# Kernel tuning notes

Measured on AMD Instinct MI355X. Metric: run time of the kernel, lower is better.

## Reference

```python
import math
import jax, jax.numpy as jnp
import numpy as np

B, T, D = 8, 2048, 512
EPS = 1e-5


def _gate(x, W, b, a, g, beta):
    # Linear -> PReLU (single shared slope a) -> LayerNorm -> sigmoid
    h = x @ W.T + b
    h = jnp.where(h >= 0, h, a * h)
    mu = jnp.mean(h, axis=-1, keepdims=True)
    var = jnp.var(h, axis=-1, keepdims=True)
    h = (h - mu) / jnp.sqrt(var + EPS) * g + beta
    return jax.nn.sigmoid(h)


def setup_inputs() -> dict:
    key = jax.random.key(0)
    ks = jax.random.split(key, 12)
    lin = lambda k: jax.random.normal(k, (D, D), jnp.float32) * 0.02
    z = jnp.zeros((D,), jnp.float32)
    o = jnp.ones((D,), jnp.float32)
    a0 = jnp.float32(0.25)  # PReLU default init
    inp = {
        "query": jax.random.normal(ks[0], (B, T, D), jnp.float32),
        "value": jax.random.normal(ks[1], (B, T, D), jnp.float32),
        "aux_emb": jax.random.normal(ks[2], (B, 1, D), jnp.float32),
        # ragged valid lengths in [T//2, T] to keep every sample realistic
        "input_len": jax.random.randint(ks[3], (B,), T // 2, T + 1),
        "Wq": lin(ks[4]), "bq": z,
        "Wqg": lin(ks[5]), "bqg": z, "aq": a0, "gq": o, "betaq": z,
        "Wkg": lin(ks[6]), "bkg": z, "ak": a0, "gk": o, "betak": z,
        "Wvg": lin(ks[7]), "bvg": z, "av": a0, "gv": o, "betav": z,
        "Wsig": lin(ks[8]), "bsig": z,
        "Wtan": lin(ks[9]), "btan": z,
    }
    return inp


def reference(query, value, aux_emb, input_len,
              Wq, bq,
              Wqg, bqg, aq, gq, betaq,
              Wkg, bkg, ak, gk, betak,
              Wvg, bvg, av, gv, betav,
              Wsig, bsig, Wtan, btan):
    q = query @ Wq.T + bq
    q = q * _gate(aux_emb, Wqg, bqg, aq, gq, betaq)          # [B,T,D]
    k = value * _gate(aux_emb, Wkg, bkg, ak, gk, betak)      # [B,T,D]
    vg = _gate(aux_emb, Wvg, bvg, av, gv, betav)             # [B,1,D]
    vg = jax.nn.sigmoid(vg @ Wsig.T + bsig) * jnp.tanh(vg @ Wtan.T + btan)
    v = value * vg                                           # [B,T,D]

    w = jnp.einsum('btd,bsd->bts', q, k) / math.sqrt(D)      # [B,T,T]
    r = jnp.arange(T)
    causal = (r[:, None] >= r[None, :]).astype(w.dtype)      # tril ones
    w = w * causal
    w = jnp.where(w == 0.0, -jnp.inf, w)  # torch quirk: exact zeros -> -inf
    L = input_len[:, None, None]                              # [B,1,1]
    invalid = (r[None, :, None] < L) & (r[None, None, :] >= L)
    w = jnp.where(invalid, -jnp.inf, w)
    p = jax.nn.softmax(w, axis=-1)
    # rows beyond input_len are padding: zero them (torch code produced NaN
    # there via -inf*0; intended semantics is zeroed padding rows)
    row_valid = (r[None, :, None] < L).astype(p.dtype)        # [B,T,1]
    p = p * row_valid
    return p @ v                                              # [B,T,D]
```

## Files before the change

kernel.cpp:

```cpp
#include <hip/hip_runtime.h>
#include <hip/hip_bf16.h>
#include <stdint.h>

#define BB 8
#define TT 2048
#define DD 512

typedef __attribute__((ext_vector_type(8))) __bf16 bf16x8;
typedef __attribute__((ext_vector_type(4))) float f32x4;
typedef __attribute__((ext_vector_type(8))) unsigned short ushort8_t;

__device__ __forceinline__ unsigned short f2bf(float f) {
    unsigned u = __builtin_bit_cast(unsigned, f);
    unsigned r = u + 0x7fffu + ((u >> 16) & 1u);
    return (unsigned short)(r >> 16);
}

__device__ __forceinline__ void gload_lds16(const unsigned short* g, unsigned short* l) {
    __builtin_amdgcn_global_load_lds(
        (const __attribute__((address_space(1))) void*)g,
        (__attribute__((address_space(3))) void*)l, 16, 0, 0);
}

__global__ __launch_bounds__(256) void gates_mv1(
    const float* __restrict__ aux,
    const float* __restrict__ Wqg, const float* __restrict__ bqg, const float* __restrict__ aq,
    const float* __restrict__ Wkg, const float* __restrict__ bkg, const float* __restrict__ ak,
    const float* __restrict__ Wvg, const float* __restrict__ bvg, const float* __restrict__ av,
    float* __restrict__ h) {
    __shared__ float saux[BB * DD];
    int tid = threadIdx.x;
#pragma unroll
    for (int i = 0; i < 4; i++) {
        int idx = tid + i * 256;
        ((float4*)saux)[idx] = ((const float4*)aux)[idx];
    }
    __syncthreads();
    int wave = (blockIdx.x * 256 + tid) >> 6;
    int lane = tid & 63;
    int g = wave >> 9, r = wave & 511;
    const float* W    = (g == 0) ? Wqg : (g == 1) ? Wkg : Wvg;
    const float* bias = (g == 0) ? bqg : (g == 1) ? bkg : bvg;
    const float* alpha = (g == 0) ? aq : (g == 1) ? ak : av;
    const float4* Wrow = (const float4*)(W + (size_t)r * DD);
    float acc[BB];
#pragma unroll
    for (int b = 0; b < BB; b++) acc[b] = 0.f;
#pragma unroll
    for (int c = 0; c < 2; c++) {
        float4 w4 = Wrow[lane + c * 64];
#pragma unroll
        for (int b = 0; b < BB; b++) {
            float4 a4 = ((const float4*)(saux + b * DD))[lane + c * 64];
            acc[b] += w4.x * a4.x + w4.y * a4.y + w4.z * a4.z + w4.w * a4.w;
        }
    }
#pragma unroll
    for (int b = 0; b < BB; b++) {
#pragma unroll
        for (int s = 1; s < 64; s <<= 1) acc[b] += __shfl_xor(acc[b], s, 64);
    }
    if (lane == 0) {
        float bi = bias[r], a = alpha[0];
#pragma unroll
        for (int b = 0; b < BB; b++) {
            float v = acc[b] + bi;
            v = (v >= 0.f) ? v : a * v;
            h[(g * BB + b) * DD + r] = v;
        }
    }
}

__global__ __launch_bounds__(512) void gates_norm(
    const float* __restrict__ h,
    const float* __restrict__ gq, const float* __restrict__ betaq,
    const float* __restrict__ gk, const float* __restrict__ betak,
    const float* __restrict__ gv, const float* __restrict__ betav,
    float* __restrict__ qgate, float* __restrict__ kgate, float* __restrict__ vg) {
    int g = blockIdx.x >> 3, b = blockIdx.x & 7, tid = threadIdx.x;
    __shared__ float red[DD], red2[DD];
    float hv = h[(g * BB + b) * DD + tid];
    red[tid] = hv; red2[tid] = hv * hv;
    __syncthreads();
    for (int s = 256; s > 0; s >>= 1) {
        if (tid < s) { red[tid] += red[tid + s]; red2[tid] += red2[tid + s]; }
        __syncthreads();
    }
    float mu = red[0] * (1.f / DD);
    float var = red2[0] * (1.f / DD) - mu * mu;
    const float* gg = (g == 0) ? gq : (g == 1) ? gk : gv;
    const float* be = (g == 0) ? betaq : (g == 1) ? betak : betav;
    float val = (hv - mu) * rsqrtf(var + 1e-5f) * gg[tid] + be[tid];
    float sg = 1.f / (1.f + expf(-val));
    float* outp = (g == 0) ? qgate : (g == 1) ? kgate : vg;
    outp[b * DD + tid] = sg;
}

__global__ __launch_bounds__(256) void gates_mv2(
    const float* __restrict__ vg,
    const float* __restrict__ Wsig, const float* __restrict__ bsig,
    const float* __restrict__ Wtan, const float* __restrict__ btan,
    float* __restrict__ vgate) {
    __shared__ float svg[BB * DD];
    int tid = threadIdx.x;
#pragma unroll
    for (int i = 0; i < 4; i++) {
        int idx = tid + i * 256;
        ((float4*)svg)[idx] = ((const float4*)vg)[idx];
    }
    __syncthreads();
    int r = (blockIdx.x * 256 + tid) >> 6;
    int lane = tid & 63;
    const float4* Ws = (const float4*)(Wsig + (size_t)r * DD);
    const float4* Wt = (const float4*)(Wtan + (size_t)r * DD);
    float as_[BB], at_[BB];
#pragma unroll
    for (int b = 0; b < BB; b++) { as_[b] = 0.f; at_[b] = 0.f; }
#pragma unroll
    for (int c = 0; c < 2; c++) {
        float4 w1 = Ws[lane + c * 64];
        float4 w2 = Wt[lane + c * 64];
#pragma unroll
        for (int b = 0; b < BB; b++) {
            float4 a4 = ((const float4*)(svg + b * DD))[lane + c * 64];
            as_[b] += w1.x * a4.x + w1.y * a4.y + w1.z * a4.z + w1.w * a4.w;
            at_[b] += w2.x * a4.x + w2.y * a4.y + w2.z * a4.z + w2.w * a4.w;
        }
    }
#pragma unroll
    for (int b = 0; b < BB; b++) {
#pragma unroll
        for (int s = 1; s < 64; s <<= 1) {
            as_[b] += __shfl_xor(as_[b], s, 64);
            at_[b] += __shfl_xor(at_[b], s, 64);
        }
    }
    if (lane == 0) {
        float b1 = bsig[r], b2 = btan[r];
#pragma unroll
        for (int b = 0; b < BB; b++) {
            float s1 = 1.f / (1.f + expf(-(as_[b] + b1)));
            float s2 = tanhf(at_[b] + b2);
            vgate[b * DD + r] = s1 * s2;
        }
    }
}

__global__ __launch_bounds__(256) void convert_kernel(
    const float* __restrict__ query, const float* __restrict__ Wq,
    const float* __restrict__ value,
    const float* __restrict__ kgate, const float* __restrict__ vgate,
    unsigned short* __restrict__ queryb, unsigned short* __restrict__ Wqb,
    unsigned short* __restrict__ kb, unsigned short* __restrict__ vbT) {
    __shared__ float tileF[64][65];
    int bi = blockIdx.x, tid = threadIdx.x;
    if (bi < 8192) {
        int idx = bi * 256 + tid;
        float4 q4 = ((const float4*)query)[idx];
        ushort4 oq;
        oq.x = f2bf(q4.x); oq.y = f2bf(q4.y); oq.z = f2bf(q4.z); oq.w = f2bf(q4.w);
        ((ushort4*)queryb)[idx] = oq;
    } else if (bi < 8448) {
        int idx = (bi - 8192) * 256 + tid;
        float4 w4 = ((const float4*)Wq)[idx];
        ushort4 o;
        o.x = f2bf(w4.x); o.y = f2bf(w4.y); o.z = f2bf(w4.z); o.w = f2bf(w4.w);
        ((ushort4*)Wqb)[idx] = o;
    } else {
        int vb = bi - 8448;
        int tIdx = vb & 31, dIdx = (vb >> 5) & 7, b = vb >> 8;
        int t0 = tIdx * 64, d0 = dIdx * 64;
        int row = tid >> 2;
        int cg = tid & 3;
        float v[16], kgv[16];
        const float* src = &value[((size_t)b * TT + t0 + row) * DD + d0 + cg * 16];
#pragma unroll
        for (int j = 0; j < 4; j++) {
            float4 f = ((const float4*)src)[j];
            v[j * 4 + 0] = f.x; v[j * 4 + 1] = f.y; v[j * 4 + 2] = f.z; v[j * 4 + 3] = f.w;
            float4 g = *(const float4*)&kgate[b * DD + d0 + cg * 16 + j * 4];
            kgv[j * 4 + 0] = g.x; kgv[j * 4 + 1] = g.y; kgv[j * 4 + 2] = g.z; kgv[j * 4 + 3] = g.w;
        }
        ushort8_t kb8[2];
#pragma unroll
        for (int h = 0; h < 2; h++)
#pragma unroll
            for (int j = 0; j < 8; j++)
                kb8[h][j] = f2bf(v[h * 8 + j] * kgv[h * 8 + j]);
        unsigned short* kdst = &kb[((size_t)b * TT + t0 + row) * DD + d0 + cg * 16];
        *(ushort8_t*)&kdst[0] = kb8[0];
        *(ushort8_t*)&kdst[8] = kb8[1];
#pragma unroll
        for (int j = 0; j < 16; j++) tileF[row][cg * 16 + j] = v[j];
        __syncthreads();
        int d = row;
        float g = vgate[b * DD + d0 + d];
        ushort8_t o8[2];
#pragma unroll
        for (int h = 0; h < 2; h++)
#pragma unroll
            for (int j = 0; j < 8; j++)
                o8[h][j] = f2bf(tileF[cg * 16 + h * 8 + j][d] * g);
        unsigned short* vdst = &vbT[((size_t)b * DD + d0 + d) * TT + t0 + cg * 16];
        *(ushort8_t*)&vdst[0] = o8[0];
        *(ushort8_t*)&vdst[8] = o8[1];
    }
}

#define STAGE_AB(BUF, K0)                                                                 \
    _Pragma("unroll") for (int i = 0; i < 2; i++) {                                       \
        int idx = tid * 8 + i * 2048;                                                     \
        int r = idx >> 5;                                                                 \
        int cg = ((idx >> 3) & 3) ^ ((r >> 1) & 3);                                       \
        gload_lds16(&Ap_[(size_t)r * lda_ + (K0) + cg * 8], &As[BUF][idx]);               \
        gload_lds16(&Bp_[(size_t)r * ldb_ + (K0) + cg * 8], &Bs[BUF][idx]);               \
    }

#define GEMM_CORE(APTR, ALDA, BPTR, BLDA, KSTART, KEND)                                   \
    __shared__ __align__(16) unsigned short As[2][128 * 32];                              \
    __shared__ __align__(16) unsigned short Bs[2][128 * 32];                              \
    const unsigned short* Ap_ = (APTR);                                                   \
    const unsigned short* Bp_ = (BPTR);                                                   \
    const int lda_ = (ALDA), ldb_ = (BLDA);                                               \
    int tid = threadIdx.x;                                                                \
    int lane = tid & 63, wid = tid >> 6;                                                  \
    int wm = (wid >> 1) * 64, wn = (wid & 1) * 64;                                        \
    int lm = lane & 15, quad = lane >> 4;                                                 \
    f32x4 acc[4][4];                                                                      \
    _Pragma("unroll") for (int im = 0; im < 4; im++)                                      \
        _Pragma("unroll") for (int in = 0; in < 4; in++)                                  \
            acc[im][in] = (f32x4){0.f, 0.f, 0.f, 0.f};                                    \
    STAGE_AB(0, (KSTART))                                                                 \
    int cur_ = 0;                                                                         \
    for (int k0 = (KSTART); k0 < (KEND); k0 += 32) {                                      \
        __syncthreads();                                                                  \
        if (k0 + 32 < (KEND)) { STAGE_AB(cur_ ^ 1, k0 + 32) }                             \
        bf16x8 af[4], bf_[4];                                                             \
        _Pragma("unroll") for (int i = 0; i < 4; i++) {                                   \
            int row = wm + i * 16 + lm;                                                   \
            af[i] = *(const bf16x8*)&As[cur_][row * 32 + (quad ^ ((row >> 1) & 3)) * 8];  \
        }                                                                                 \
        _Pragma("unroll") for (int i = 0; i < 4; i++) {                                   \
            int row = wn + i * 16 + lm;                                                   \
            bf_[i] = *(const bf16x8*)&Bs[cur_][row * 32 + (quad ^ ((row >> 1) & 3)) * 8]; \
        }                                                                                 \
        _Pragma("unroll") for (int im = 0; im < 4; im++)                                  \
            _Pragma("unroll") for (int in = 0; in < 4; in++)                              \
                acc[im][in] = __builtin_amdgcn_mfma_f32_16x16x32_bf16(af[im], bf_[in],    \
                                                                     acc[im][in], 0, 0, 0);\
        cur_ ^= 1;                                                                        \
    }

__global__ __launch_bounds__(256) void qgemm_kernel(
    const unsigned short* __restrict__ Amat, const unsigned short* __restrict__ Bmat,
    const float* __restrict__ bq, const float* __restrict__ qgate,
    unsigned short* __restrict__ qb) {
    int m0 = blockIdx.x * 128, n0 = blockIdx.y * 128;
    const unsigned short* Ap = Amat + (size_t)m0 * DD;
    const unsigned short* Bp = Bmat + (size_t)n0 * DD;
    GEMM_CORE(Ap, DD, Bp, DD, 0, DD)
    int b = m0 >> 11;
#pragma unroll
    for (int im = 0; im < 4; im++) {
        int row = m0 + wm + im * 16 + quad * 4;
#pragma unroll
        for (int in = 0; in < 4; in++) {
            int col = n0 + wn + in * 16 + lm;
            float bias = bq[col];
            float g = qgate[b * DD + col];
#pragma unroll
            for (int r = 0; r < 4; r++) {
                float v = (acc[im][in][r] + bias) * g;
                qb[(size_t)(row + r) * DD + col] = f2bf(v);
            }
        }
    }
}

__global__ __launch_bounds__(256) void scores_kernel(
    const unsigned short* __restrict__ qb, const unsigned short* __restrict__ kb,
    unsigned short* __restrict__ P, float* __restrict__ rowsum) {
    int b = blockIdx.z;
    int idx = blockIdx.x;
    int mt = (int)((sqrtf(8.f * idx + 1.f) - 1.f) * 0.5f);
    while ((mt + 1) * (mt + 2) / 2 <= idx) mt++;
    while (mt * (mt + 1) / 2 > idx) mt--;
    int nt = idx - mt * (mt + 1) / 2;
    int t0 = mt * 128, s0 = nt * 128;
    const unsigned short* Ap = qb + ((size_t)b * TT + t0) * DD;
    const unsigned short* Bp = kb + ((size_t)b * TT + s0) * DD;
    GEMM_CORE(Ap, DD, Bp, DD, 0, DD)
    const float scale = 0.044194173824159216f;
    unsigned short* Ptile = P + ((size_t)b * 136 + (size_t)mt * (mt + 1) / 2 + nt) * 16384;
#pragma unroll
    for (int im = 0; im < 4; im++) {
        int ltb = wm + im * 16 + quad * 4;
        float rs[4] = {0.f, 0.f, 0.f, 0.f};
#pragma unroll
        for (int in = 0; in < 4; in++) {
            int ls = wn + in * 16 + lm;
            int s = s0 + ls;
#pragma unroll
            for (int r = 0; r < 4; r++) {
                float p = (s <= t0 + ltb + r) ? expf(acc[im][in][r] * scale) : 0.f;
                Ptile[(size_t)(ltb + r) * 128 + ls] = f2bf(p);
                rs[r] += p;
            }
        }
#pragma unroll
        for (int r = 0; r < 4; r++) {
            float v = rs[r];
            v += __shfl_xor(v, 1, 64);
            v += __shfl_xor(v, 2, 64);
            v += __shfl_xor(v, 4, 64);
            v += __shfl_xor(v, 8, 64);
            if (lm == 0) atomicAdd(&rowsum[b * TT + t0 + ltb + r], v);
        }
    }
}

__global__ __launch_bounds__(256) void out_kernel(
    const unsigned short* __restrict__ P, const unsigned short* __restrict__ vbT,
    const float* __restrict__ rowsum, const int* __restrict__ input_len,
    float* __restrict__ out) {
    int lin = blockIdx.x + 4 * blockIdx.y + 64 * blockIdx.z;
    int b = lin & 7;
    int rem = lin >> 3;
    int nt = rem & 3;
    int pr = rem >> 2;
    int n0 = nt * 128;
    int L = input_len[b];

    __shared__ __align__(16) unsigned short As[2][64 * 64];
    __shared__ __align__(16) unsigned short Bs[2][128 * 64];
    int tid = threadIdx.x;
    int lane = tid & 63, wid = tid >> 6;
    int wm = (wid >> 1) * 32, wn = (wid & 1) * 64;
    int lm = lane & 15, quad = lane >> 4;

#pragma unroll
    for (int half = 0; half < 2; half++) {
        int mt = half ? (31 - pr) : pr;
        int t0 = mt * 64;
        int mt128 = mt >> 1;
        int rowoff = (mt & 1) * 64;
        size_t triBase = ((size_t)b * 136 + (size_t)mt128 * (mt128 + 1) / 2) * 16384;
        int ksteps = mt + 1;

        f32x4 acc[2][4];
#pragma unroll
        for (int im = 0; im < 2; im++)
#pragma unroll
            for (int in = 0; in < 4; in++) acc[im][in] = (f32x4){0.f, 0.f, 0.f, 0.f};

#define OUT_STAGE(BUF, KS)                                                              \
        {                                                                               \
            int k0s = (KS) * 64;                                                        \
            int stile = k0s >> 7;                                                       \
            int coloff = k0s & 64;                                                      \
            _Pragma("unroll") for (int i = 0; i < 2; i++) {                             \
                int idx = tid * 8 + i * 2048;                                           \
                int r = idx >> 6;                                                       \
                int c = (idx >> 3) & 7;                                                 \
                int cs = c ^ (r & 7);                                                   \
                const unsigned short* ag = P + triBase + (size_t)stile * 16384 +        \
                                           (size_t)(rowoff + r) * 128 + coloff + cs * 8;\
                gload_lds16(ag, &As[BUF][idx]);                                         \
            }                                                                           \
            _Pragma("unroll") for (int i = 0; i < 4; i++) {                             \
                int idx = tid * 8 + i * 2048;                                           \
                int r = idx >> 6;                                                       \
                int c = (idx >> 3) & 7;                                                 \
                int cs = c ^ (r & 7);                                                   \
                gload_lds16(&vbT[(size_t)(b * DD + n0 + r) * TT + k0s + cs * 8],        \
                            &Bs[BUF][idx]);                                             \
            }                                                                           \
        }

        OUT_STAGE(0, 0)
        int cur = 0;
        for (int ks = 0; ks < ksteps; ks++) {
            __syncthreads();
            if (ks + 1 < ksteps) { OUT_STAGE(cur ^ 1, ks + 1) }
            bf16x8 af[2][2], bf_[4][2];
#pragma unroll
            for (int kk = 0; kk < 2; kk++) {
#pragma unroll
                for (int i = 0; i < 2; i++) {
                    int row = wm + i * 16 + lm;
                    af[i][kk] = *(const bf16x8*)&As[cur][row * 64 + ((kk * 4 + quad) ^ (row & 7)) * 8];
                }
#pragma unroll
                for (int i = 0; i < 4; i++) {
                    int row = wn + i * 16 + lm;
                    bf_[i][kk] = *(const bf16x8*)&Bs[cur][row * 64 + ((kk * 4 + quad) ^ (row & 7)) * 8];
                }
            }
#pragma unroll
            for (int kk = 0; kk < 2; kk++)
#pragma unroll
                for (int im = 0; im < 2; im++)
#pragma unroll
                    for (int in = 0; in < 4; in++)
                        acc[im][in] = __builtin_amdgcn_mfma_f32_16x16x32_bf16(
                            af[im][kk], bf_[in][kk], acc[im][in], 0, 0, 0);
            cur ^= 1;
        }
        __syncthreads();
#undef OUT_STAGE

#pragma unroll
        for (int im = 0; im < 2; im++) {
            int tbase = t0 + wm + im * 16 + quad * 4;
#pragma unroll
            for (int r = 0; r < 4; r++) {
                int t = tbase + r;
                float inv = 1.f / rowsum[b * TT + t];
                bool valid = (t < L);
#pragma unroll
                for (int in = 0; in < 4; in++) {
                    int n = n0 + wn + in * 16 + lm;
                    float o = valid ? acc[im][in][r] * inv : 0.f;
                    out[((size_t)b * TT + t) * DD + n] = o;
                }
            }
        }
    }
}

extern "C" void kernel_launch(void* const* d_in, const int* in_sizes, int n_in,
                              void* d_out, int out_size, void* d_ws, size_t ws_size,
                              hipStream_t stream) {
    const float* query = (const float*)d_in[0];
    const float* value = (const float*)d_in[1];
    const float* aux   = (const float*)d_in[2];
    const int*   ilen  = (const int*)d_in[3];
    const float* Wq    = (const float*)d_in[4];
    const float* bq    = (const float*)d_in[5];
    const float* Wqg   = (const float*)d_in[6];
    const float* bqg   = (const float*)d_in[7];
    const float* aq    = (const float*)d_in[8];
    const float* gq    = (const float*)d_in[9];
    const float* betaq = (const float*)d_in[10];
    const float* Wkg   = (const float*)d_in[11];
    const float* bkg   = (const float*)d_in[12];
    const float* ak    = (const float*)d_in[13];
    const float* gk    = (const float*)d_in[14];
    const float* betak = (const float*)d_in[15];
    const float* Wvg   = (const float*)d_in[16];
    const float* bvg   = (const float*)d_in[17];
    const float* av    = (const float*)d_in[18];
    const float* gv    = (const float*)d_in[19];
    const float* betav = (const float*)d_in[20];
    const float* Wsig  = (const float*)d_in[21];
    const float* bsig  = (const float*)d_in[22];
    const float* Wtan  = (const float*)d_in[23];
    const float* btan  = (const float*)d_in[24];

    char* ws = (char*)d_ws;
    float* qgate          = (float*)(ws + 0);
    float* kgate          = (float*)(ws + 16384);
    float* vgate          = (float*)(ws + 32768);
    float* rowsum         = (float*)(ws + 49152);
    unsigned short* Wqb   = (unsigned short*)(ws + 114688);
    unsigned short* queryb= (unsigned short*)(ws + 638976);
    unsigned short* qb    = (unsigned short*)(ws + 17416192);
    unsigned short* kb    = (unsigned short*)(ws + 34193408);
    unsigned short* vbT   = (unsigned short*)(ws + 50970624);
    unsigned short* P     = (unsigned short*)(ws + 67747840);
    float* hbuf           = (float*)(ws + 67747840);
    float* vg             = (float*)(ws + 67747840 + 49152);

    hipMemsetAsync(rowsum, 0, BB * TT * sizeof(float), stream);

    gates_mv1<<<384, 256, 0, stream>>>(aux, Wqg, bqg, aq, Wkg, bkg, ak, Wvg, bvg, av, hbuf);
    gates_norm<<<24, 512, 0, stream>>>(hbuf, gq, betaq, gk, betak, gv, betav,
                                       qgate, kgate, vg);
    gates_mv2<<<128, 256, 0, stream>>>(vg, Wsig, bsig, Wtan, btan, vgate);

    convert_kernel<<<10496, 256, 0, stream>>>(query, Wq, value, kgate, vgate,
                                              queryb, Wqb, kb, vbT);
    qgemm_kernel<<<dim3((BB * TT) / 128, DD / 128), 256, 0, stream>>>(queryb, Wqb, bq, qgate, qb);
    scores_kernel<<<dim3(136, 1, BB), 256, 0, stream>>>(qb, kb, P, rowsum);
    out_kernel<<<dim3(4, 16, BB), 256, 0, stream>>>(P, vbT, rowsum, ilen, (float*)d_out);
}
```

Before: 274.2 us.

## Fuse gate matvecs, layernorm, and rowsum zeroing into one per-batch kernel

Three gate kernels (matvec, layernorm/sigmoid, second matvec) and the rowsum memset are merged into one kernel with one 512-thread block per batch. Each thread computes a full 512-length dot product for one output row, and results pass between stages through shared memory. This removes three launches and a memset along with their intermediate global round-trips. The cost is only 8 blocks in flight, each thread streaming a whole weight row uncoalesced, and every block re-reading all five weight matrices, which may serialize gate computation.

```diff
diff --git a/kernel.cpp b/kernel.cpp
--- a/kernel.cpp
+++ b/kernel.cpp
@@ -22,128 +22,76 @@
         (__attribute__((address_space(3))) void*)l, 16, 0, 0);
 }
 
-__global__ __launch_bounds__(256) void gates_mv1(
+__global__ __launch_bounds__(512) void gates_fused(
     const float* __restrict__ aux,
     const float* __restrict__ Wqg, const float* __restrict__ bqg, const float* __restrict__ aq,
     const float* __restrict__ Wkg, const float* __restrict__ bkg, const float* __restrict__ ak,
     const float* __restrict__ Wvg, const float* __restrict__ bvg, const float* __restrict__ av,
-    float* __restrict__ h) {
-    __shared__ float saux[BB * DD];
-    int tid = threadIdx.x;
-#pragma unroll
-    for (int i = 0; i < 4; i++) {
-        int idx = tid + i * 256;
-        ((float4*)saux)[idx] = ((const float4*)aux)[idx];
-    }
-    __syncthreads();
-    int wave = (blockIdx.x * 256 + tid) >> 6;
-    int lane = tid & 63;
-    int g = wave >> 9, r = wave & 511;
-    const float* W    = (g == 0) ? Wqg : (g == 1) ? Wkg : Wvg;
-    const float* bias = (g == 0) ? bqg : (g == 1) ? bkg : bvg;
-    const float* alpha = (g == 0) ? aq : (g == 1) ? ak : av;
-    const float4* Wrow = (const float4*)(W + (size_t)r * DD);
-    float acc[BB];
-#pragma unroll
-    for (int b = 0; b < BB; b++) acc[b] = 0.f;
-#pragma unroll
-    for (int c = 0; c < 2; c++) {
-        float4 w4 = Wrow[lane + c * 64];
-#pragma unroll
-        for (int b = 0; b < BB; b++) {
-            float4 a4 = ((const float4*)(saux + b * DD))[lane + c * 64];
-            acc[b] += w4.x * a4.x + w4.y * a4.y + w4.z * a4.z + w4.w * a4.w;
-        }
-    }
-#pragma unroll
-    for (int b = 0; b < BB; b++) {
-#pragma unroll
-        for (int s = 1; s < 64; s <<= 1) acc[b] += __shfl_xor(acc[b], s, 64);
-    }
-    if (lane == 0) {
-        float bi = bias[r], a = alpha[0];
-#pragma unroll
-        for (int b = 0; b < BB; b++) {
-            float v = acc[b] + bi;
-            v = (v >= 0.f) ? v : a * v;
-            h[(g * BB + b) * DD + r] = v;
-        }
-    }
-}
-
-__global__ __launch_bounds__(512) void gates_norm(
-    const float* __restrict__ h,
     const float* __restrict__ gq, const float* __restrict__ betaq,
     const float* __restrict__ gk, const float* __restrict__ betak,
     const float* __restrict__ gv, const float* __restrict__ betav,
-    float* __restrict__ qgate, float* __restrict__ kgate, float* __restrict__ vg) {
-    int g = blockIdx.x >> 3, b = blockIdx.x & 7, tid = threadIdx.x;
-    __shared__ float red[DD], red2[DD];
-    float hv = h[(g * BB + b) * DD + tid];
-    red[tid] = hv; red2[tid] = hv * hv;
-    __syncthreads();
-    for (int s = 256; s > 0; s >>= 1) {
-        if (tid < s) { red[tid] += red[tid + s]; red2[tid] += red2[tid + s]; }
-        __syncthreads();
-    }
-    float mu = red[0] * (1.f / DD);
-    float var = red2[0] * (1.f / DD) - mu * mu;
-    const float* gg = (g == 0) ? gq : (g == 1) ? gk : gv;
-    const float* be = (g == 0) ? betaq : (g == 1) ? betak : betav;
-    float val = (hv - mu) * rsqrtf(var + 1e-5f) * gg[tid] + be[tid];
-    float sg = 1.f / (1.f + expf(-val));
-    float* outp = (g == 0) ? qgate : (g == 1) ? kgate : vg;
-    outp[b * DD + tid] = sg;
-}
-
-__global__ __launch_bounds__(256) void gates_mv2(
-    const float* __restrict__ vg,
     const float* __restrict__ Wsig, const float* __restrict__ bsig,
     const float* __restrict__ Wtan, const float* __restrict__ btan,
-    float* __restrict__ vgate) {
-    __shared__ float svg[BB * DD];
-    int tid = threadIdx.x;
-#pragma unroll
-    for (int i = 0; i < 4; i++) {
-        int idx = tid + i * 256;
-        ((float4*)svg)[idx] = ((const float4*)vg)[idx];
-    }
+    float* __restrict__ qgate, float* __restrict__ kgate, float* __restrict__ vgate,
+    float* __restrict__ rowsum) {
+    int b = blockIdx.x, tid = threadIdx.x;
+    __shared__ float saux[DD];
+    __shared__ float red[DD], red2[DD];
+    __shared__ float vgsh[DD];
+
+#pragma unroll
+    for (int i = 0; i < 4; i++) rowsum[b * TT + tid + i * 512] = 0.f;
+
+    if (tid < 128) ((float4*)saux)[tid] = ((const float4*)(aux + (size_t)b * DD))[tid];
     __syncthreads();
-    int r = (blockIdx.x * 256 + tid) >> 6;
-    int lane = tid & 63;
-    const float4* Ws = (const float4*)(Wsig + (size_t)r * DD);
-    const float4* Wt = (const float4*)(Wtan + (size_t)r * DD);
-    float as_[BB], at_[BB];
-#pragma unroll
-    for (int b = 0; b < BB; b++) { as_[b] = 0.f; at_[b] = 0.f; }
-#pragma unroll
-    for (int c = 0; c < 2; c++) {
-        float4 w1 = Ws[lane + c * 64];
-        float4 w2 = Wt[lane + c * 64];
-#pragma unroll
-        for (int b = 0; b < BB; b++) {
-            float4 a4 = ((const float4*)(svg + b * DD))[lane + c * 64];
-            as_[b] += w1.x * a4.x + w1.y * a4.y + w1.z * a4.z + w1.w * a4.w;
-            at_[b] += w2.x * a4.x + w2.y * a4.y + w2.z * a4.z + w2.w * a4.w;
-        }
-    }
-#pragma unroll
-    for (int b = 0; b < BB; b++) {
-#pragma unroll
-        for (int s = 1; s < 64; s <<= 1) {
-            as_[b] += __shfl_xor(as_[b], s, 64);
-            at_[b] += __shfl_xor(at_[b], s, 64);
-        }
-    }
-    if (lane == 0) {
-        float b1 = bsig[r], b2 = btan[r];
-#pragma unroll
-        for (int b = 0; b < BB; b++) {
-            float s1 = 1.f / (1.f + expf(-(as_[b] + b1)));
-            float s2 = tanhf(at_[b] + b2);
-            vgate[b * DD + r] = s1 * s2;
-        }
-    }
+
+#pragma unroll 1
+    for (int g = 0; g < 3; g++) {
+        const float* W     = (g == 0) ? Wqg : (g == 1) ? Wkg : Wvg;
+        const float* bias  = (g == 0) ? bqg : (g == 1) ? bkg : bvg;
+        const float* alpha = (g == 0) ? aq  : (g == 1) ? ak  : av;
+        const float4* Wrow = (const float4*)(W + (size_t)tid * DD);
+        float acc = 0.f;
+#pragma unroll 8
+        for (int c = 0; c < 128; c++) {
+            float4 w4 = Wrow[c];
+            float4 a4 = ((const float4*)saux)[c];
+            acc += w4.x * a4.x + w4.y * a4.y + w4.z * a4.z + w4.w * a4.w;
+        }
+        float v = acc + bias[tid];
+        v = (v >= 0.f) ? v : alpha[0] * v;
+        red[tid] = v; red2[tid] = v * v;
+        __syncthreads();
+        for (int s = 256; s > 0; s >>= 1) {
+            if (tid < s) { red[tid] += red[tid + s]; red2[tid] += red2[tid + s]; }
+            __syncthreads();
+        }
+        float mu  = red[0] * (1.f / DD);
+        float var = red2[0] * (1.f / DD) - mu * mu;
+        const float* gg = (g == 0) ? gq : (g == 1) ? gk : gv;
+        const float* be = (g == 0) ? betaq : (g == 1) ? betak : betav;
+        float val = (v - mu) * rsqrtf(var + 1e-5f) * gg[tid] + be[tid];
+        float sg = 1.f / (1.f + expf(-val));
+        if (g == 0)      qgate[b * DD + tid] = sg;
+        else if (g == 1) kgate[b * DD + tid] = sg;
+        else             vgsh[tid] = sg;
+        __syncthreads();
+    }
+
+    const float4* Ws = (const float4*)(Wsig + (size_t)tid * DD);
+    const float4* Wt = (const float4*)(Wtan + (size_t)tid * DD);
+    float as_ = 0.f, at_ = 0.f;
+#pragma unroll 8
+    for (int c = 0; c < 128; c++) {
+        float4 a4 = ((const float4*)vgsh)[c];
+        float4 w1 = Ws[c];
+        float4 w2 = Wt[c];
+        as_ += w1.x * a4.x + w1.y * a4.y + w1.z * a4.z + w1.w * a4.w;
+        at_ += w2.x * a4.x + w2.y * a4.y + w2.z * a4.z + w2.w * a4.w;
+    }
+    float s1 = 1.f / (1.f + expf(-(as_ + bsig[tid])));
+    float s2 = tanhf(at_ + btan[tid]);
+    vgate[b * DD + tid] = s1 * s2;
 }
 
 __global__ __launch_bounds__(256) void convert_kernel(
@@ -468,15 +416,12 @@
     unsigned short* kb    = (unsigned short*)(ws + 34193408);
     unsigned short* vbT   = (unsigned short*)(ws + 50970624);
     unsigned short* P     = (unsigned short*)(ws + 67747840);
-    float* hbuf           = (float*)(ws + 67747840);
-    float* vg             = (float*)(ws + 67747840 + 49152);
-
-    hipMemsetAsync(rowsum, 0, BB * TT * sizeof(float), stream);
-
-    gates_mv1<<<384, 256, 0, stream>>>(aux, Wqg, bqg, aq, Wkg, bkg, ak, Wvg, bvg, av, hbuf);
-    gates_norm<<<24, 512, 0, stream>>>(hbuf, gq, betaq, gk, betak, gv, betav,
-                                       qgate, kgate, vg);
-    gates_mv2<<<128, 256, 0, stream>>>(vg, Wsig, bsig, Wtan, btan, vgate);
+
+    gates_fused<<<BB, 512, 0, stream>>>(aux,
+                                        Wqg, bqg, aq, Wkg, bkg, ak, Wvg, bvg, av,
+                                        gq, betaq, gk, betak, gv, betav,
+                                        Wsig, bsig, Wtan, btan,
+                                        qgate, kgate, vgate, rowsum);
 
     convert_kernel<<<10496, 256, 0, stream>>>(query, Wq, value, kgate, vgate,
                                               queryb, Wqb, kb, vbT);
```

Measured after the change: 425.0 us. 55.0% more time.
